# Optimization experiments

Hardware: AMD Instinct MI355X
Metric: run time of the kernel (lower is better)

## Reference

```python
import jax, jax.numpy as jnp
import numpy as np

# Irrep structure (fixed by init_kwargs):
#   irreps_in      = 128x0e + 128x1o          -> x: [N, 128 + 128*3] = [N, 512]
#   irreps_nonlin  = 32x0e + 16x1o            (16 scalars + 16 gates + 16 gated vectors)
#   hidden_irreps  = 16x0e + 16x1o            (Gate output)
#   irreps_out     = 10x0e + 1x1o             -> out: [N, 13]
MUL_IN = 128
N_SCAL = 16   # gated-block scalars
N_GATE = 16   # gate scalars
N_VEC = 16    # gated 1o multiplicity
NUM_ELEM = 10


def setup_inputs() -> dict:
    key = jax.random.key(0)
    ks = jax.random.split(key, 8)
    N = 100000
    x = jax.random.normal(ks[0], (N, MUL_IN * 4), dtype=jnp.float32)  # 128 scalars + 128 vectors
    # o3.Linear weights: N(0,1) init, one (mul_in, mul_out) block per matching irrep pair
    W1_s = jax.random.normal(ks[1], (MUL_IN, N_SCAL + N_GATE), dtype=jnp.float32)  # 128x0e -> 32x0e
    W1_v = jax.random.normal(ks[2], (MUL_IN, N_VEC), dtype=jnp.float32)            # 128x1o -> 16x1o
    b1_s = jax.random.normal(ks[3], (N_SCAL + N_GATE,), dtype=jnp.float32) * 0.1   # bias on 0e only
    W2_s = jax.random.normal(ks[4], (N_SCAL, NUM_ELEM), dtype=jnp.float32)         # 16x0e -> 10x0e
    W2_v = jax.random.normal(ks[5], (N_VEC, 1), dtype=jnp.float32)                 # 16x1o -> 1x1o
    b2_s = jax.random.normal(ks[6], (NUM_ELEM,), dtype=jnp.float32) * 0.1
    return {"x": x, "W1_s": W1_s, "W1_v": W1_v, "b1_s": b1_s,
            "W2_s": W2_s, "W2_v": W2_v, "b2_s": b2_s}


def reference(x, W1_s, W1_v, b1_s, W2_s, W2_v, b2_s):
    N = x.shape[0]
    inv1 = 1.0 / np.sqrt(MUL_IN)   # o3.Linear path normalization (single path per output)
    inv2s = 1.0 / np.sqrt(N_SCAL)
    inv2v = 1.0 / np.sqrt(N_VEC)

    x_s = x[:, :MUL_IN]                               # [N, 128] scalars (0e)
    x_v = x[:, MUL_IN:].reshape(N, MUL_IN, 3)         # [N, 128, 3] vectors (1o)

    # linear_1: irreps_in -> irreps_nonlin (bias on scalar outputs only)
    h_s = x_s @ W1_s * inv1 + b1_s                    # [N, 32]
    h_v = jnp.einsum('nic,io->noc', x_v, W1_v) * inv1 # [N, 16, 3]

    # Gate: silu on scalars; silu(gates) elementwise-scales gated vectors
    scalars = jax.nn.silu(h_s[:, :N_SCAL])            # [N, 16]
    gates = jax.nn.silu(h_s[:, N_SCAL:])              # [N, 16]
    gated_v = gates[:, :, None] * h_v                 # [N, 16, 3]

    # linear_2: hidden_irreps -> irreps_out (10x0e + 1x1o)
    out_s = scalars @ W2_s * inv2s + b2_s             # [N, 10]
    out_v = jnp.einsum('nic,io->noc', gated_v, W2_v) * inv2v  # [N, 1, 3]
    return jnp.concatenate([out_s, out_v.reshape(N, 3)], axis=-1)  # [N, 13]
```

## Files before the change

### kernel.cpp

```cpp
#include <hip/hip_runtime.h>
#include <math.h>


typedef short  bf16x8 __attribute__((ext_vector_type(8)));
typedef int    i32x4  __attribute__((ext_vector_type(4)));
typedef float  f32x4  __attribute__((ext_vector_type(4)));

static __device__ __forceinline__ short f2bf(float f) {
    union { float f; unsigned u; } v; v.f = f;
    return (short)((v.u + 0x8000u) >> 16);
}
static __device__ __forceinline__ unsigned cvtpk(float lo, float hi) {
    unsigned r;
    asm("v_cvt_pk_bf16_f32 %0, %1, %2" : "=v"(r) : "v"(lo), "v"(hi));
    return r;
}

#define BLOCK 256

__global__ __launch_bounds__(BLOCK, 2) void nlrb_kernel(
    const float* __restrict__ x,
    const float* __restrict__ W1s,
    const float* __restrict__ W1v,
    const float* __restrict__ b1s,
    const float* __restrict__ W2s,
    const float* __restrict__ W2v,
    const float* __restrict__ b2s,
    float* __restrict__ out,
    int N)
{
    __shared__ float sred[4][16][68];

    const int tid  = threadIdx.x;
    const int wave = tid >> 6;
    const int lane = tid & 63;
    const int mq   = lane >> 4;
    const int o    = lane & 15;
    const float inv1 = 0.08838834764831843f;

    bf16x8 bS0[4], bS1[4], bV[4];
    #pragma unroll
    for (int kb = 0; kb < 4; ++kb) {
        #pragma unroll
        for (int j = 0; j < 8; ++j) {
            const int k = kb * 32 + mq * 8 + j;
            bS0[kb][j] = f2bf(W1s[k * 32 + o]);
            bS1[kb][j] = f2bf(W1s[k * 32 + 16 + o]);
            bV [kb][j] = f2bf(W1v[k * 16 + o]);
        }
    }
    float wcr[16];
    #pragma unroll
    for (int j = 0; j < 16; ++j)
        wcr[j] = (o < 10) ? W2s[j * 10 + o] : W2v[j];
    const float b2e = (o < 10) ? b2s[o] : 0.0f;
    const float b1a = b1s[o];
    const float b1b = b1s[16 + o];

    const int NT = N >> 4;
    const int wstride = gridDim.x << 2;
    const int wt0 = (blockIdx.x << 2) + wave;

    float4 LS[4][2], LV[4][6];

#define ISSUE_S(kb, xp)                                                      \
    do {                                                                     \
        LS[kb][0] = *(const float4*)((xp) + (kb) * 32 + mq * 8);             \
        LS[kb][1] = *(const float4*)((xp) + (kb) * 32 + mq * 8 + 4);         \
    } while (0)
#define ISSUE_V(kb, xp)                                                      \
    do {                                                                     \
        _Pragma("unroll")                                                    \
        for (int q = 0; q < 6; ++q)                                          \
            LV[kb][q] = *(const float4*)((xp) + 128 + (kb) * 96 + mq * 24 + q * 4); \
    } while (0)

#define TILE_BODY(PF)                                                        \
    do {                                                                     \
        f32x4 accS0 = {0.f,0.f,0.f,0.f}, accS1 = {0.f,0.f,0.f,0.f};          \
        f32x4 accV0 = {0.f,0.f,0.f,0.f}, accV1 = {0.f,0.f,0.f,0.f};          \
        f32x4 accV2 = {0.f,0.f,0.f,0.f};                                     \
                 \
        _Pragma("unroll")                                                    \
        for (int kb = 0; kb < 4; ++kb) {                                     \
            i32x4 wv;                                                        \
            wv[0] = (int)cvtpk(LS[kb][0].x, LS[kb][0].y);                    \
            wv[1] = (int)cvtpk(LS[kb][0].z, LS[kb][0].w);                    \
            wv[2] = (int)cvtpk(LS[kb][1].x, LS[kb][1].y);                    \
            wv[3] = (int)cvtpk(LS[kb][1].z, LS[kb][1].w);                    \
            if (PF) ISSUE_S(kb, xq);                                         \
            const bf16x8 a = __builtin_bit_cast(bf16x8, wv);                 \
            accS0 = __builtin_amdgcn_mfma_f32_16x16x32_bf16(a, bS0[kb], accS0, 0, 0, 0); \
            accS1 = __builtin_amdgcn_mfma_f32_16x16x32_bf16(a, bS1[kb], accS1, 0, 0, 0); \
        }                                                                    \
           \
        _Pragma("unroll")                                                    \
        for (int kb = 0; kb < 4; ++kb) {                                     \
            unsigned p[12];                                                  \
            _Pragma("unroll")                                                \
            for (int q = 0; q < 6; ++q) {                                    \
                p[2*q]   = cvtpk(LV[kb][q].x, LV[kb][q].y);                  \
                p[2*q+1] = cvtpk(LV[kb][q].z, LV[kb][q].w);                  \
            }                                                                \
            if (PF) ISSUE_V(kb, xq);                                         \
            i32x4 w0, w1, w2;                                                \
            _Pragma("unroll")                                                \
            for (int w = 0; w < 4; ++w) {                                    \
                w0[w] = (int)__builtin_amdgcn_perm(p[3*w+1], p[3*w],   0x07060100u); \
                w1[w] = (int)__builtin_amdgcn_perm(p[3*w+2], p[3*w],   0x05040302u); \
                w2[w] = (int)__builtin_amdgcn_perm(p[3*w+2], p[3*w+1], 0x07060100u); \
            }                                                                \
            const bf16x8 a0 = __builtin_bit_cast(bf16x8, w0);                \
            const bf16x8 a1 = __builtin_bit_cast(bf16x8, w1);                \
            const bf16x8 a2 = __builtin_bit_cast(bf16x8, w2);                \
            accV0 = __builtin_amdgcn_mfma_f32_16x16x32_bf16(a0, bV[kb], accV0, 0, 0, 0); \
            accV1 = __builtin_amdgcn_mfma_f32_16x16x32_bf16(a1, bV[kb], accV1, 0, 0, 0); \
            accV2 = __builtin_amdgcn_mfma_f32_16x16x32_bf16(a2, bV[kb], accV2, 0, 0, 0); \
        }                                                                    \
                             \
        _Pragma("unroll")                                                    \
        for (int v = 0; v < 4; ++v) {                                        \
            const float hs = fmaf(accS0[v], inv1, b1a);                      \
            const float hg = fmaf(accS1[v], inv1, b1b);                      \
            const float s  = hs / (1.f + __expf(-hs));                       \
            const float g  = hg / (1.f + __expf(-hg));                       \
            const float gm = g * inv1;                                       \
            const int  r   = mq * 4 + v;                                     \
            sred[wave][r][o]      = s;                                       \
            sred[wave][r][16 + o] = gm * accV0[v];                           \
            sred[wave][r][32 + o] = gm * accV1[v];                           \
            sred[wave][r][48 + o] = gm * accV2[v];                           \
        }                                                                    \
        asm volatile("s_waitcnt lgkmcnt(0)" ::: "memory");                   \
              \
        _Pragma("unroll")                                                    \
        for (int w = 0; w < 4; ++w) {                                        \
            const int r = (w << 2) + mq;                                     \
            if (o < 13) {                                                    \
                const int slot = (o < 10) ? 0 : (o - 9);                     \
                const float* sp = &sred[wave][r][slot * 16];                 \
                float sum = 0.f;                                             \
                _Pragma("unroll")                                            \
                for (int q = 0; q < 4; ++q) {                                \
                    const float4 pv = *(const float4*)(sp + q * 4);          \
                    sum = fmaf(pv.x, wcr[q * 4 + 0], sum);                   \
                    sum = fmaf(pv.y, wcr[q * 4 + 1], sum);                   \
                    sum = fmaf(pv.z, wcr[q * 4 + 2], sum);                   \
                    sum = fmaf(pv.w, wcr[q * 4 + 3], sum);                   \
                }                                                            \
                out[(size_t)(base + r) * 13 + o] = fmaf(sum, 0.25f, b2e);    \
            }                                                                \
        }                                                                    \
        asm volatile("s_waitcnt lgkmcnt(0)" ::: "memory");                   \
    } while (0)

    if (wt0 < NT) {
        const float* xp = x + (size_t)((wt0 << 4) + o) * 512;
        #pragma unroll
        for (int kb = 0; kb < 4; ++kb) { ISSUE_S(kb, xp); ISSUE_V(kb, xp); }
    }

    int wt = wt0;
    for (; wt + wstride < NT; wt += wstride) {
        const int base = wt << 4;
        const float* xq = x + (size_t)(((wt + wstride) << 4) + o) * 512;
        TILE_BODY(1);
    }
    if (wt < NT) {
        const int base = wt << 4;
        const float* xq = nullptr; (void)xq;
        TILE_BODY(0);
    }
#undef ISSUE_S
#undef ISSUE_V
#undef TILE_BODY
}

extern "C" void kernel_launch(void* const* d_in, const int* in_sizes, int n_in,
                              void* d_out, int out_size, void* d_ws, size_t ws_size,
                              hipStream_t stream) {
    const float* x   = (const float*)d_in[0];
    const float* W1s = (const float*)d_in[1];
    const float* W1v = (const float*)d_in[2];
    const float* b1s = (const float*)d_in[3];
    const float* W2s = (const float*)d_in[4];
    const float* W2v = (const float*)d_in[5];
    const float* b2s = (const float*)d_in[6];
    float* outp = (float*)d_out;
    const int N = in_sizes[0] / 512;
    nlrb_kernel<<<dim3(512), dim3(BLOCK), 0, stream>>>(
        x, W1s, W1v, b1s, W2s, W2v, b2s, outp, N);
}
```

Baseline: 40.33 us.

## Compute second linear layer with MFMA instead of LDS reduction

Swaps the A/B operands of the first-layer MFMAs so the accumulator layout puts hidden features along the register dimension. The second linear layer (scalars, and gated vectors per component) then becomes two extra bf16 MFMAs against packed W2 fragments, with the bias folded into the accumulator. This removes the shared-memory staging, LDS waits and per-lane scalar FMA reduction. The cost is that the second-layer inputs are rounded to bf16, which adds precision loss.

```diff
diff --git a/kernel.cpp b/kernel.cpp
--- a/kernel.cpp
+++ b/kernel.cpp
@@ -17,6 +17,7 @@
 }
 
 #define BLOCK 256
+#define MFMA32(a, b, c) __builtin_amdgcn_mfma_f32_16x16x32_bf16(a, b, c, 0, 0, 0)
 
 __global__ __launch_bounds__(BLOCK, 2) void nlrb_kernel(
     const float* __restrict__ x,
@@ -29,13 +30,11 @@
     float* __restrict__ out,
     int N)
 {
-    __shared__ float sred[4][16][68];
-
     const int tid  = threadIdx.x;
     const int wave = tid >> 6;
     const int lane = tid & 63;
-    const int mq   = lane >> 4;
-    const int o    = lane & 15;
+    const int q    = lane >> 4;
+    const int rw   = lane & 15;
     const float inv1 = 0.08838834764831843f;
 
     bf16x8 bS0[4], bS1[4], bV[4];
@@ -43,19 +42,31 @@
     for (int kb = 0; kb < 4; ++kb) {
         #pragma unroll
         for (int j = 0; j < 8; ++j) {
-            const int k = kb * 32 + mq * 8 + j;
-            bS0[kb][j] = f2bf(W1s[k * 32 + o]);
-            bS1[kb][j] = f2bf(W1s[k * 32 + 16 + o]);
-            bV [kb][j] = f2bf(W1v[k * 16 + o]);
+            const int k = kb * 32 + q * 8 + j;
+            bS0[kb][j] = f2bf(W1s[k * 32 + rw]);
+            bS1[kb][j] = f2bf(W1s[k * 32 + 16 + rw]);
+            bV [kb][j] = f2bf(W1v[k * 16 + rw]);
         }
     }
-    float wcr[16];
+
+    float b1sv[4], b1gv[4], b2v4[4];
     #pragma unroll
-    for (int j = 0; j < 16; ++j)
-        wcr[j] = (o < 10) ? W2s[j * 10 + o] : W2v[j];
-    const float b2e = (o < 10) ? b2s[o] : 0.0f;
-    const float b1a = b1s[o];
-    const float b1b = b1s[16 + o];
+    for (int v = 0; v < 4; ++v) {
+        const int j = q * 4 + v;
+        b1sv[v] = b1s[j];
+        b1gv[v] = b1s[16 + j];
+        b2v4[v] = (j < 10) ? b2s[j] * 4.0f : 0.0f;
+    }
+
+    bf16x8 a2A, a2B;
+    #pragma unroll
+    for (int j = 0; j < 8; ++j) {
+        const int o = q * 4 + (j & 3);
+        a2A[j] = f2bf((j < 4) ? ((rw < 10)  ? W2s[o * 10 + rw] : 0.0f)
+                              : ((rw == 10) ? W2v[o] : 0.0f));
+        a2B[j] = f2bf((j < 4) ? ((rw == 11) ? W2v[o] : 0.0f)
+                              : ((rw == 12) ? W2v[o] : 0.0f));
+    }
 
     const int NT = N >> 4;
     const int wstride = gridDim.x << 2;
@@ -65,14 +76,14 @@
 
 #define ISSUE_S(kb, xp)                                                      \
     do {                                                                     \
-        LS[kb][0] = *(const float4*)((xp) + (kb) * 32 + mq * 8);             \
-        LS[kb][1] = *(const float4*)((xp) + (kb) * 32 + mq * 8 + 4);         \
+        LS[kb][0] = *(const float4*)((xp) + (kb) * 32 + q * 8);              \
+        LS[kb][1] = *(const float4*)((xp) + (kb) * 32 + q * 8 + 4);          \
     } while (0)
 #define ISSUE_V(kb, xp)                                                      \
     do {                                                                     \
         _Pragma("unroll")                                                    \
-        for (int q = 0; q < 6; ++q)                                          \
-            LV[kb][q] = *(const float4*)((xp) + 128 + (kb) * 96 + mq * 24 + q * 4); \
+        for (int qq = 0; qq < 6; ++qq)                                       \
+            LV[kb][qq] = *(const float4*)((xp) + 128 + (kb) * 96 + q * 24 + qq * 4); \
     } while (0)
 
 #define TILE_BODY(PF)                                                        \
@@ -80,7 +91,7 @@
         f32x4 accS0 = {0.f,0.f,0.f,0.f}, accS1 = {0.f,0.f,0.f,0.f};          \
         f32x4 accV0 = {0.f,0.f,0.f,0.f}, accV1 = {0.f,0.f,0.f,0.f};          \
         f32x4 accV2 = {0.f,0.f,0.f,0.f};                                     \
-                 \
+                          \
         _Pragma("unroll")                                                    \
         for (int kb = 0; kb < 4; ++kb) {                                     \
             i32x4 wv;                                                        \
@@ -90,17 +101,16 @@
             wv[3] = (int)cvtpk(LS[kb][1].z, LS[kb][1].w);                    \
             if (PF) ISSUE_S(kb, xq);                                         \
             const bf16x8 a = __builtin_bit_cast(bf16x8, wv);                 \
-            accS0 = __builtin_amdgcn_mfma_f32_16x16x32_bf16(a, bS0[kb], accS0, 0, 0, 0); \
-            accS1 = __builtin_amdgcn_mfma_f32_16x16x32_bf16(a, bS1[kb], accS1, 0, 0, 0); \
+            accS0 = MFMA32(bS0[kb], a, accS0);                               \
+            accS1 = MFMA32(bS1[kb], a, accS1);                               \
         }                                                                    \
-           \
         _Pragma("unroll")                                                    \
         for (int kb = 0; kb < 4; ++kb) {                                     \
             unsigned p[12];                                                  \
             _Pragma("unroll")                                                \
-            for (int q = 0; q < 6; ++q) {                                    \
-                p[2*q]   = cvtpk(LV[kb][q].x, LV[kb][q].y);                  \
-                p[2*q+1] = cvtpk(LV[kb][q].z, LV[kb][q].w);                  \
+            for (int qq = 0; qq < 6; ++qq) {                                 \
+                p[2*qq]   = cvtpk(LV[kb][qq].x, LV[kb][qq].y);               \
+                p[2*qq+1] = cvtpk(LV[kb][qq].z, LV[kb][qq].w);               \
             }                                                                \
             if (PF) ISSUE_V(kb, xq);                                         \
             i32x4 w0, w1, w2;                                                \
@@ -113,49 +123,42 @@
             const bf16x8 a0 = __builtin_bit_cast(bf16x8, w0);                \
             const bf16x8 a1 = __builtin_bit_cast(bf16x8, w1);                \
             const bf16x8 a2 = __builtin_bit_cast(bf16x8, w2);                \
-            accV0 = __builtin_amdgcn_mfma_f32_16x16x32_bf16(a0, bV[kb], accV0, 0, 0, 0); \
-            accV1 = __builtin_amdgcn_mfma_f32_16x16x32_bf16(a1, bV[kb], accV1, 0, 0, 0); \
-            accV2 = __builtin_amdgcn_mfma_f32_16x16x32_bf16(a2, bV[kb], accV2, 0, 0, 0); \
+            accV0 = MFMA32(bV[kb], a0, accV0);                               \
+            accV1 = MFMA32(bV[kb], a1, accV1);                               \
+            accV2 = MFMA32(bV[kb], a2, accV2);                               \
         }                                                                    \
-                             \
+          \
+        float sv[4], g0[4], g1[4], g2[4];                                    \
         _Pragma("unroll")                                                    \
         for (int v = 0; v < 4; ++v) {                                        \
-            const float hs = fmaf(accS0[v], inv1, b1a);                      \
-            const float hg = fmaf(accS1[v], inv1, b1b);                      \
+            const float hs = fmaf(accS0[v], inv1, b1sv[v]);                  \
+            const float hg = fmaf(accS1[v], inv1, b1gv[v]);                  \
             const float s  = hs / (1.f + __expf(-hs));                       \
             const float g  = hg / (1.f + __expf(-hg));                       \
             const float gm = g * inv1;                                       \
-            const int  r   = mq * 4 + v;                                     \
-            sred[wave][r][o]      = s;                                       \
-            sred[wave][r][16 + o] = gm * accV0[v];                           \
-            sred[wave][r][32 + o] = gm * accV1[v];                           \
-            sred[wave][r][48 + o] = gm * accV2[v];                           \
+            sv[v] = s;                                                       \
+            g0[v] = gm * accV0[v];                                           \
+            g1[v] = gm * accV1[v];                                           \
+            g2[v] = gm * accV2[v];                                           \
         }                                                                    \
-        asm volatile("s_waitcnt lgkmcnt(0)" ::: "memory");                   \
-              \
+        i32x4 bA, bB;                                                        \
+        bA[0] = (int)cvtpk(sv[0], sv[1]); bA[1] = (int)cvtpk(sv[2], sv[3]);  \
+        bA[2] = (int)cvtpk(g0[0], g0[1]); bA[3] = (int)cvtpk(g0[2], g0[3]);  \
+        bB[0] = (int)cvtpk(g1[0], g1[1]); bB[1] = (int)cvtpk(g1[2], g1[3]);  \
+        bB[2] = (int)cvtpk(g2[0], g2[1]); bB[3] = (int)cvtpk(g2[2], g2[3]);  \
+        f32x4 acc2 = {b2v4[0], b2v4[1], b2v4[2], b2v4[3]};                   \
+        acc2 = MFMA32(a2A, __builtin_bit_cast(bf16x8, bA), acc2);            \
+        acc2 = MFMA32(a2B, __builtin_bit_cast(bf16x8, bB), acc2);            \
         _Pragma("unroll")                                                    \
-        for (int w = 0; w < 4; ++w) {                                        \
-            const int r = (w << 2) + mq;                                     \
-            if (o < 13) {                                                    \
-                const int slot = (o < 10) ? 0 : (o - 9);                     \
-                const float* sp = &sred[wave][r][slot * 16];                 \
-                float sum = 0.f;                                             \
-                _Pragma("unroll")                                            \
-                for (int q = 0; q < 4; ++q) {                                \
-                    const float4 pv = *(const float4*)(sp + q * 4);          \
-                    sum = fmaf(pv.x, wcr[q * 4 + 0], sum);                   \
-                    sum = fmaf(pv.y, wcr[q * 4 + 1], sum);                   \
-                    sum = fmaf(pv.z, wcr[q * 4 + 2], sum);                   \
-                    sum = fmaf(pv.w, wcr[q * 4 + 3], sum);                   \
-                }                                                            \
-                out[(size_t)(base + r) * 13 + o] = fmaf(sum, 0.25f, b2e);    \
-            }                                                                \
+        for (int v = 0; v < 4; ++v) {                                        \
+            const int e = (q << 2) + v;                                      \
+            if (e < 13)                                                      \
+                out[(size_t)((base) + rw) * 13 + e] = acc2[v] * 0.25f;       \
         }                                                                    \
-        asm volatile("s_waitcnt lgkmcnt(0)" ::: "memory");                   \
     } while (0)
 
     if (wt0 < NT) {
-        const float* xp = x + (size_t)((wt0 << 4) + o) * 512;
+        const float* xp = x + (size_t)((wt0 << 4) + rw) * 512;
         #pragma unroll
         for (int kb = 0; kb < 4; ++kb) { ISSUE_S(kb, xp); ISSUE_V(kb, xp); }
     }
@@ -163,7 +166,7 @@
     int wt = wt0;
     for (; wt + wstride < NT; wt += wstride) {
         const int base = wt << 4;
-        const float* xq = x + (size_t)(((wt + wstride) << 4) + o) * 512;
+        const float* xq = x + (size_t)(((wt + wstride) << 4) + rw) * 512;
         TILE_BODY(1);
     }
     if (wt < NT) {
```

New measurement: 43.64 us. +8.2%, slower.
